# Kernel optimization log

Hardware: AMD Instinct MI355X
Metric: run time of the kernel (lower is better)

## Reference

```python
import jax, jax.numpy as jnp
import numpy as np

BATCH = 4096
IN_DIM = 512
OUT_DIM = 512
GRID_SIZE = 5
K = 3


def _extended_grid():
    # Original: grid = linspace(-1, 1, grid_size+1), spacing h = 2/grid_size.
    # The de Boor-Cox recursion in the source indexes up to grid[grid_size+2k],
    # so we extend the uniform grid to the right with the same spacing.
    h = 2.0 / GRID_SIZE
    return (-1.0 + h * jnp.arange(GRID_SIZE + 2 * K + 1)).astype(jnp.float32)


def bspline_basis(x, grid, k):
    """Vectorized de Boor-Cox recursion.
    x: [..., ] floats; returns basis [..., grid_size + k].
    Identical math to the recursive b_spline_basis in the source, but computed
    bottom-up over all knot intervals at once (no redundant recomputation).
    """
    xe = x[..., None]  # [..., 1]
    # degree-0: indicator of half-open knot intervals, [..., n_knots-1]
    B = ((grid[:-1] <= xe) & (xe < grid[1:])).astype(x.dtype)
    for d in range(1, k + 1):
        n = grid.shape[0] - d - 1
        gi, gid = grid[:n], grid[d:d + n]          # grid[i], grid[i+d]
        gi1, gid1 = grid[1:n + 1], grid[d + 1:d + n + 1]  # grid[i+1], grid[i+d+1]
        # uniform grid -> denominators are d*h, never zero
        B = (xe - gi) / (gid - gi) * B[..., :n] + (gid1 - xe) / (gid1 - gi1) * B[..., 1:n + 1]
    return B  # [..., grid_size + k]


def setup_inputs() -> dict:
    key = jax.random.key(0)
    k1, k2 = jax.random.split(key)
    x = jax.random.uniform(k1, (BATCH, IN_DIM), jnp.float32) * 2.0 - 1.0  # in [-1, 1)
    spline_coeff = jax.random.normal(k2, (IN_DIM, OUT_DIM, GRID_SIZE + K), jnp.float32)
    spline_scaling = jnp.ones((IN_DIM, OUT_DIM), jnp.float32)
    return {"x": x, "spline_coeff": spline_coeff, "spline_scaling": spline_scaling}


def reference(x, spline_coeff, spline_scaling):
    grid = _extended_grid()
    basis = bspline_basis(x, grid, K)  # [B, in_dim, grid_size+k]
    # out[b, j] = sum_i scaling[i,j] * sum_g basis[b,i,g] * coeff[i,j,g]
    return jnp.einsum('big,ijg,ij->bj', basis, spline_coeff, spline_scaling)
```

## Files before the change

kernel.cpp:

```cpp
#include <hip/hip_runtime.h>
#include <hip/hip_bf16.h>
#include <stdint.h>


#define BATCH   4096
#define IN_DIM  512
#define OUT_DIM 512
#define KDIM    (IN_DIM * 8)
#define NKT     (KDIM / 64)

typedef short short8 __attribute__((ext_vector_type(8)));
typedef float f32x4  __attribute__((ext_vector_type(4)));

#define W_VM12_LG0 0x07C

__device__ __forceinline__ unsigned int f2bf(float f) {
  union { float f; unsigned int u; } v; v.f = f;
  unsigned int r = v.u + 0x7FFFu + ((v.u >> 16) & 1u);
  return r >> 16;
}

__device__ __forceinline__ short8 basis_pack8(float xv) {
  float t = __builtin_fmaf(xv, 2.5f, 2.5f);
  int m = (int)t;
  m = m > 4 ? 4 : m;
  float u  = t - (float)m;
  float u2 = u * u, u3 = u2 * u, om = 1.0f - u;
  float om2 = om * om;
  float w0 = om2 * om * (1.0f / 6.0f);
  float w1 = __builtin_fmaf(u3, 0.5f, __builtin_fmaf(u2, -1.0f, 2.0f / 3.0f));
  float s  = (u2 - u3) + u;
  float w2 = __builtin_fmaf(s, 0.5f, 1.0f / 6.0f);
  float w3 = u3 * (1.0f / 6.0f);
  unsigned d0 = __builtin_amdgcn_perm(__float_as_uint(w1), __float_as_uint(w0), 0x07060302u);
  unsigned d1 = __builtin_amdgcn_perm(__float_as_uint(w3), __float_as_uint(w2), 0x07060302u);
  uint64_t wp = ((uint64_t)d1 << 32) | d0;
  int sh = m * 16 - 48;
  uint64_t lo = (sh >= 0) ? (wp << sh) : (wp >> (-sh));
  unsigned hi = (sh > 0) ? (unsigned)(wp >> (64 - sh)) : 0u;
  union { unsigned d[4]; short8 s8; } r;
  r.d[0] = (unsigned)lo; r.d[1] = (unsigned)(lo >> 32); r.d[2] = hi; r.d[3] = 0u;
  return r.s8;
}

__device__ __forceinline__ void async_load16(const void* g, void* l) {
  __builtin_amdgcn_global_load_lds(
      (__attribute__((address_space(1))) void*)(uintptr_t)g,
      (__attribute__((address_space(3))) void*)(unsigned int)(uintptr_t)l,
      16, 0, 0);
}

__global__ void kan_prep(const float* __restrict__ coeff,
                         const float* __restrict__ scaling,
                         unsigned short* __restrict__ Wt) {
  int idx = blockIdx.x * 256 + threadIdx.x;
  int i = idx >> 9, j = idx & 511;
  float s = scaling[idx];
  const float4* cp = reinterpret_cast<const float4*>(coeff) + (size_t)idx * 2;
  float4 c0 = cp[0], c1 = cp[1];
  short8 h;
  h[0] = (short)f2bf(c0.x * s); h[1] = (short)f2bf(c0.y * s);
  h[2] = (short)f2bf(c0.z * s); h[3] = (short)f2bf(c0.w * s);
  h[4] = (short)f2bf(c1.x * s); h[5] = (short)f2bf(c1.y * s);
  h[6] = (short)f2bf(c1.z * s); h[7] = (short)f2bf(c1.w * s);
  *reinterpret_cast<short8*>(Wt + (size_t)j * KDIM + i * 8) = h;
}

__global__ __launch_bounds__(256, 2)
void kan_gemm_r(const float* __restrict__ x,
                const unsigned short* __restrict__ Wt,
                float* __restrict__ out) {
  __shared__ unsigned short Bs[4][64 * 64];

  const int tid  = threadIdx.x;
  const int lane = tid & 63;
  const int wid  = tid >> 6;
  const int ln = lane & 15, quad = lane >> 4;

  const int b    = blockIdx.x;
  const int row0 = (b & 31) * 128;
  const int col0 = (b >> 5) * 64;

  f32x4 acc[2][4] = {};

  const int lr = lane >> 3;
  const int cg = (lane & 7) ^ lr;
  const unsigned short* bP0 = Wt + (size_t)(col0 + wid * 16 + lr) * KDIM + cg * 8;
  const unsigned short* bP1 = bP0 + (size_t)8 * KDIM;

  const float* xP0 = x + (size_t)(row0 + wid * 32 + ln) * IN_DIM + quad;
  const float* xP1 = xP0 + (size_t)16 * IN_DIM;

  int boff[2][4];
#pragma unroll
  for (int kk = 0; kk < 2; ++kk)
#pragma unroll
    for (int nt = 0; nt < 4; ++nt) {
      const int c = nt * 16 + ln;
      boff[kk][nt] = c * 64 + (((kk * 4 + quad) ^ (c & 7)) * 8);
    }

  auto issueB = [&](int kt, int st) {
    const int k0 = kt * 64;
    async_load16(bP0 + k0, &Bs[st][(wid * 16) * 64]);
    async_load16(bP1 + k0, &Bs[st][(wid * 16 + 8) * 64]);
  };

  float xa[2][2][2];
  auto loadx = [&](int t, int buf) {
#pragma unroll
    for (int kk = 0; kk < 2; ++kk) {
      xa[buf][0][kk] = xP0[t * 8 + kk * 4];
      xa[buf][1][kk] = xP1[t * 8 + kk * 4];
    }
  };

  issueB(0, 0);
  issueB(1, 1);
  loadx(0, 0);
  issueB(2, 2);
  loadx(1, 1);

  for (int g = 0; g < 16; ++g) {
#pragma unroll
    for (int s = 0; s < 4; ++s) {
      const int kt = g * 4 + s;
      __builtin_amdgcn_s_waitcnt(W_VM12_LG0);
      __builtin_amdgcn_s_barrier();
      float cur[2][2];
#pragma unroll
      for (int mt = 0; mt < 2; ++mt)
#pragma unroll
        for (int kk = 0; kk < 2; ++kk) cur[mt][kk] = xa[s & 1][mt][kk];
      const int kb = (kt + 3 < NKT) ? kt + 3 : NKT - 1;
      const int kx = (kt + 2 < NKT) ? kt + 2 : NKT - 1;
      issueB(kb, (s + 3) & 3);
      loadx(kx, s & 1);
#pragma unroll
      for (int kk = 0; kk < 2; ++kk) {
        short8 af0 = basis_pack8(cur[0][kk]);
        short8 af1 = basis_pack8(cur[1][kk]);
#pragma unroll
        for (int nt = 0; nt < 4; ++nt) {
          short8 bfr = *reinterpret_cast<const short8*>(&Bs[s][boff[kk][nt]]);
          acc[0][nt] = __builtin_amdgcn_mfma_f32_16x16x32_bf16(af0, bfr, acc[0][nt], 0, 0, 0);
          acc[1][nt] = __builtin_amdgcn_mfma_f32_16x16x32_bf16(af1, bfr, acc[1][nt], 0, 0, 0);
        }
      }
    }
  }

#pragma unroll
  for (int mt = 0; mt < 2; ++mt)
#pragma unroll
    for (int nt = 0; nt < 4; ++nt) {
      const int col = col0 + nt * 16 + ln;
#pragma unroll
      for (int r = 0; r < 4; ++r) {
        const int row = row0 + wid * 32 + mt * 16 + quad * 4 + r;
        out[(size_t)row * OUT_DIM + col] = acc[mt][nt][r];
      }
    }
}

__global__ __launch_bounds__(256, 2)
void kan_gemm_fb(const float* __restrict__ x, const float* __restrict__ coeff,
                 const float* __restrict__ scaling, float* __restrict__ out) {
  __shared__ unsigned short As[64 * 64];
  __shared__ unsigned short Bs[64 * 64];

  const int tid  = threadIdx.x;
  const int lane = tid & 63;
  const int wid  = tid >> 6;
  const int wm = wid >> 1, wn = wid & 1;
  const int ln = lane & 15, quad = lane >> 4;
  const int row0 = blockIdx.y * 64;
  const int col0 = blockIdx.x * 64;

  f32x4 acc[2][2] = {};

  for (int kt = 0; kt < KDIM / 64; ++kt) {
#pragma unroll
    for (int pp = 0; pp < 2; ++pp) {
      const int p  = tid + pp * 256;
      const int rn = p & 63;
      const int il = p >> 6;
      const int sw = ((il ^ (rn & 7)) * 8);
      short8 ha = basis_pack8(x[(size_t)(row0 + rn) * IN_DIM + kt * 8 + il]);
      *reinterpret_cast<short8*>(&As[rn * 64 + sw]) = ha;
      const float* cbase = coeff + (size_t)(kt * 8 + il) * 4096 + (size_t)(col0 + rn) * 8;
      float4 c0 = reinterpret_cast<const float4*>(cbase)[0];
      float4 c1 = reinterpret_cast<const float4*>(cbase)[1];
      float s = scaling[(size_t)(kt * 8 + il) * OUT_DIM + col0 + rn];
      short8 hb;
      hb[0] = (short)f2bf(c0.x * s); hb[1] = (short)f2bf(c0.y * s);
      hb[2] = (short)f2bf(c0.z * s); hb[3] = (short)f2bf(c0.w * s);
      hb[4] = (short)f2bf(c1.x * s); hb[5] = (short)f2bf(c1.y * s);
      hb[6] = (short)f2bf(c1.z * s); hb[7] = (short)f2bf(c1.w * s);
      *reinterpret_cast<short8*>(&Bs[rn * 64 + sw]) = hb;
    }
    __syncthreads();
#pragma unroll
    for (int kk = 0; kk < 2; ++kk) {
      short8 af[2], bfr[2];
#pragma unroll
      for (int mt = 0; mt < 2; ++mt) {
        const int r  = wm * 32 + mt * 16 + ln;
        const int pc = (kk * 4 + quad) ^ (r & 7);
        af[mt] = *reinterpret_cast<const short8*>(&As[r * 64 + pc * 8]);
      }
#pragma unroll
      for (int nt = 0; nt < 2; ++nt) {
        const int c  = wn * 32 + nt * 16 + ln;
        const int pc = (kk * 4 + quad) ^ (c & 7);
        bfr[nt] = *reinterpret_cast<const short8*>(&Bs[c * 64 + pc * 8]);
      }
#pragma unroll
      for (int mt = 0; mt < 2; ++mt)
#pragma unroll
        for (int nt = 0; nt < 2; ++nt)
          acc[mt][nt] = __builtin_amdgcn_mfma_f32_16x16x32_bf16(af[mt], bfr[nt], acc[mt][nt], 0, 0, 0);
    }
    __syncthreads();
  }
#pragma unroll
  for (int mt = 0; mt < 2; ++mt)
#pragma unroll
    for (int nt = 0; nt < 2; ++nt) {
      const int col = col0 + wn * 32 + nt * 16 + ln;
#pragma unroll
      for (int r = 0; r < 4; ++r) {
        const int row = row0 + wm * 32 + mt * 16 + quad * 4 + r;
        out[(size_t)row * OUT_DIM + col] = acc[mt][nt][r];
      }
    }
}

extern "C" void kernel_launch(void* const* d_in, const int* in_sizes, int n_in,
                              void* d_out, int out_size, void* d_ws, size_t ws_size,
                              hipStream_t stream) {
  const float* x       = (const float*)d_in[0];
  const float* coeff   = (const float*)d_in[1];
  const float* scaling = (const float*)d_in[2];
  float* out = (float*)d_out;

  const size_t needW = (size_t)OUT_DIM * KDIM * 2;

  if (ws_size >= needW) {
    unsigned short* Wt = (unsigned short*)d_ws;
    kan_prep<<<(IN_DIM * OUT_DIM) / 256, 256, 0, stream>>>(coeff, scaling, Wt);
    kan_gemm_r<<<(BATCH / 128) * (OUT_DIM / 64), 256, 0, stream>>>(x, Wt, out);
  } else {
    kan_gemm_fb<<<dim3(OUT_DIM / 64, BATCH / 64), 256, 0, stream>>>(x, coeff, scaling, out);
  }
}
```

Before: 120.7 us.

## Stage x through LDS with async loads and shrink GEMM tile to 64x64

The GEMM kernel now loads x asynchronously into a 4-stage LDS ring alongside the weight tiles, instead of reading it directly into registers. The basis expansion for the next k-step is computed after the current MFMAs so it overlaps with them. The block tile drops from 128x64 to 64x64, doubling the grid to 512 blocks, which lowers per-block work and register pressure. The cost is that each weight tile is reused by half as many rows, so weight traffic to L2 doubles.

```diff
diff --git a/kernel.cpp b/kernel.cpp
--- a/kernel.cpp
+++ b/kernel.cpp
@@ -12,7 +12,8 @@
 typedef short short8 __attribute__((ext_vector_type(8)));
 typedef float f32x4  __attribute__((ext_vector_type(4)));
 
-#define W_VM12_LG0 0x07C
+#define W_VM8  0xF78
+#define W_VM12 0xF7C
 
 __device__ __forceinline__ unsigned int f2bf(float f) {
   union { float f; unsigned int u; } v; v.f = f;
@@ -49,6 +50,12 @@
       (__attribute__((address_space(3))) void*)(unsigned int)(uintptr_t)l,
       16, 0, 0);
 }
+__device__ __forceinline__ void async_load4(const void* g, void* l) {
+  __builtin_amdgcn_global_load_lds(
+      (__attribute__((address_space(1))) void*)(uintptr_t)g,
+      (__attribute__((address_space(3))) void*)(unsigned int)(uintptr_t)l,
+      4, 0, 0);
+}
 
 __global__ void kan_prep(const float* __restrict__ coeff,
                          const float* __restrict__ scaling,
@@ -67,10 +74,11 @@
 }
 
 __global__ __launch_bounds__(256, 2)
-void kan_gemm_r(const float* __restrict__ x,
-                const unsigned short* __restrict__ Wt,
-                float* __restrict__ out) {
+void kan_gemm_ra(const float* __restrict__ x,
+                 const unsigned short* __restrict__ Wt,
+                 float* __restrict__ out) {
   __shared__ unsigned short Bs[4][64 * 64];
+  __shared__ float          Xs[4][512];
 
   const int tid  = threadIdx.x;
   const int lane = tid & 63;
@@ -78,18 +86,22 @@
   const int ln = lane & 15, quad = lane >> 4;
 
   const int b    = blockIdx.x;
-  const int row0 = (b & 31) * 128;
-  const int col0 = (b >> 5) * 64;
-
-  f32x4 acc[2][4] = {};
+  const int row0 = (b & 63) * 64;
+  const int col0 = (b >> 6) * 64;
+
+  f32x4 acc[4] = {};
 
   const int lr = lane >> 3;
   const int cg = (lane & 7) ^ lr;
   const unsigned short* bP0 = Wt + (size_t)(col0 + wid * 16 + lr) * KDIM + cg * 8;
   const unsigned short* bP1 = bP0 + (size_t)8 * KDIM;
 
-  const float* xP0 = x + (size_t)(row0 + wid * 32 + ln) * IN_DIM + quad;
-  const float* xP1 = xP0 + (size_t)16 * IN_DIM;
+  const int f0 = wid * 128 + lane;
+  const int f1 = f0 + 64;
+  const float* xG0 = x + (size_t)(row0 + (f0 >> 3)) * IN_DIM + (f0 & 7);
+  const float* xG1 = x + (size_t)(row0 + (f1 >> 3)) * IN_DIM + (f1 & 7);
+
+  const int xoff = (wid * 16 + ln) * 8 + quad;
 
   int boff[2][4];
 #pragma unroll
@@ -105,62 +117,57 @@
     async_load16(bP0 + k0, &Bs[st][(wid * 16) * 64]);
     async_load16(bP1 + k0, &Bs[st][(wid * 16 + 8) * 64]);
   };
-
-  float xa[2][2][2];
-  auto loadx = [&](int t, int buf) {
-#pragma unroll
-    for (int kk = 0; kk < 2; ++kk) {
-      xa[buf][0][kk] = xP0[t * 8 + kk * 4];
-      xa[buf][1][kk] = xP1[t * 8 + kk * 4];
-    }
+  auto issueX = [&](int kt, int st) {
+    async_load4(xG0 + kt * 8, &Xs[st][wid * 128]);
+    async_load4(xG1 + kt * 8, &Xs[st][wid * 128 + 64]);
   };
 
-  issueB(0, 0);
-  issueB(1, 1);
-  loadx(0, 0);
-  issueB(2, 2);
-  loadx(1, 1);
+  issueX(0, 0); issueB(0, 0);
+  issueX(1, 1); issueB(1, 1);
+  issueX(2, 2); issueB(2, 2);
+  issueX(3, 3);
+  __builtin_amdgcn_s_waitcnt(W_VM12);
+  __builtin_amdgcn_s_barrier();
+  short8 afc0, afc1;
+  { float xv0 = Xs[0][xoff], xv1 = Xs[0][xoff + 4];
+    afc0 = basis_pack8(xv0); afc1 = basis_pack8(xv1); }
 
   for (int g = 0; g < 16; ++g) {
 #pragma unroll
     for (int s = 0; s < 4; ++s) {
       const int kt = g * 4 + s;
-      __builtin_amdgcn_s_waitcnt(W_VM12_LG0);
+      __builtin_amdgcn_s_waitcnt(W_VM8);
       __builtin_amdgcn_s_barrier();
-      float cur[2][2];
-#pragma unroll
-      for (int mt = 0; mt < 2; ++mt)
-#pragma unroll
-        for (int kk = 0; kk < 2; ++kk) cur[mt][kk] = xa[s & 1][mt][kk];
+      float xv0 = Xs[(s + 1) & 3][xoff];
+      float xv1 = Xs[(s + 1) & 3][xoff + 4];
       const int kb = (kt + 3 < NKT) ? kt + 3 : NKT - 1;
-      const int kx = (kt + 2 < NKT) ? kt + 2 : NKT - 1;
+      const int kx = (kt + 4 < NKT) ? kt + 4 : NKT - 1;
       issueB(kb, (s + 3) & 3);
-      loadx(kx, s & 1);
-#pragma unroll
-      for (int kk = 0; kk < 2; ++kk) {
-        short8 af0 = basis_pack8(cur[0][kk]);
-        short8 af1 = basis_pack8(cur[1][kk]);
-#pragma unroll
-        for (int nt = 0; nt < 4; ++nt) {
-          short8 bfr = *reinterpret_cast<const short8*>(&Bs[s][boff[kk][nt]]);
-          acc[0][nt] = __builtin_amdgcn_mfma_f32_16x16x32_bf16(af0, bfr, acc[0][nt], 0, 0, 0);
-          acc[1][nt] = __builtin_amdgcn_mfma_f32_16x16x32_bf16(af1, bfr, acc[1][nt], 0, 0, 0);
-        }
-      }
-    }
-  }
-
-#pragma unroll
-  for (int mt = 0; mt < 2; ++mt)
-#pragma unroll
-    for (int nt = 0; nt < 4; ++nt) {
-      const int col = col0 + nt * 16 + ln;
-#pragma unroll
-      for (int r = 0; r < 4; ++r) {
-        const int row = row0 + wid * 32 + mt * 16 + quad * 4 + r;
-        out[(size_t)row * OUT_DIM + col] = acc[mt][nt][r];
-      }
-    }
+      issueX(kx, s);
+#pragma unroll
+      for (int nt = 0; nt < 4; ++nt) {
+        short8 b0 = *reinterpret_cast<const short8*>(&Bs[s][boff[0][nt]]);
+        acc[nt] = __builtin_amdgcn_mfma_f32_16x16x32_bf16(afc0, b0, acc[nt], 0, 0, 0);
+      }
+#pragma unroll
+      for (int nt = 0; nt < 4; ++nt) {
+        short8 b1 = *reinterpret_cast<const short8*>(&Bs[s][boff[1][nt]]);
+        acc[nt] = __builtin_amdgcn_mfma_f32_16x16x32_bf16(afc1, b1, acc[nt], 0, 0, 0);
+      }
+      afc0 = basis_pack8(xv0);
+      afc1 = basis_pack8(xv1);
+    }
+  }
+
+#pragma unroll
+  for (int nt = 0; nt < 4; ++nt) {
+    const int col = col0 + nt * 16 + ln;
+#pragma unroll
+    for (int r = 0; r < 4; ++r) {
+      const int row = row0 + wid * 16 + quad * 4 + r;
+      out[(size_t)row * OUT_DIM + col] = acc[nt][r];
+    }
+  }
 }
 
 __global__ __launch_bounds__(256, 2)
@@ -249,7 +256,7 @@
   if (ws_size >= needW) {
     unsigned short* Wt = (unsigned short*)d_ws;
     kan_prep<<<(IN_DIM * OUT_DIM) / 256, 256, 0, stream>>>(coeff, scaling, Wt);
-    kan_gemm_r<<<(BATCH / 128) * (OUT_DIM / 64), 256, 0, stream>>>(x, Wt, out);
+    kan_gemm_ra<<<(BATCH / 64) * (OUT_DIM / 64), 256, 0, stream>>>(x, Wt, out);
   } else {
     kan_gemm_fb<<<dim3(OUT_DIM / 64, BATCH / 64), 256, 0, stream>>>(x, coeff, scaling, out);
   }
```

After: 102.5 us. 1.18x faster.
